# Optimization experiments

Hardware: AMD Instinct MI355X
Metric: run time of the kernel (lower is better)

Reference implementation:

```python
import jax, jax.numpy as jnp
import numpy as np

B, S, D, H = 2, 2048, 2048, 16
DH = D // H
FF = 4 * D
EPS = 1e-5


def setup_inputs() -> dict:
    key = jax.random.key(0)
    ks = jax.random.split(key, 8)
    sd = 0.02
    return {
        "hidden_states": jax.random.normal(ks[0], (B, S, D), jnp.float32),
        "ln1_w": jnp.ones((D,), jnp.float32),
        "ln1_b": jnp.zeros((D,), jnp.float32),
        "qkv_w": jax.random.normal(ks[1], (3 * D, D), jnp.float32) * sd,
        "qkv_b": jnp.zeros((3 * D,), jnp.float32),
        "dense_w": jax.random.normal(ks[2], (D, D), jnp.float32) * sd,
        "dense_b": jnp.zeros((D,), jnp.float32),
        "ln2_w": jnp.ones((D,), jnp.float32),
        "ln2_b": jnp.zeros((D,), jnp.float32),
        "fc1_w": jax.random.normal(ks[3], (FF, D), jnp.float32) * sd,
        "fc1_b": jnp.zeros((FF,), jnp.float32),
        "fc2_w": jax.random.normal(ks[4], (D, FF), jnp.float32) * sd,
        "fc2_b": jnp.zeros((D,), jnp.float32),
    }


def _layer_norm(x, w, b):
    mu = jnp.mean(x, axis=-1, keepdims=True)
    var = jnp.mean(jnp.square(x - mu), axis=-1, keepdims=True)
    return (x - mu) * jax.lax.rsqrt(var + EPS) * w + b


def _attention(x, qkv_w, qkv_b, dense_w, dense_b):
    qkv = x @ qkv_w.T + qkv_b  # [B,S,3D]
    q, k, v = jnp.split(qkv, 3, axis=-1)
    q = q.reshape(B, S, H, DH)
    k = k.reshape(B, S, H, DH)
    v = v.reshape(B, S, H, DH)
    scale = DH ** -0.5
    scores = jnp.einsum("bqhd,bkhd->bhqk", q, k) * scale
    causal = jnp.tril(jnp.ones((S, S), bool))
    scores = jnp.where(causal, scores, jnp.finfo(scores.dtype).min)
    probs = jax.nn.softmax(scores, axis=-1)
    out = jnp.einsum("bhqk,bkhd->bqhd", probs, v).reshape(B, S, D)
    return out @ dense_w.T + dense_b


def reference(hidden_states, ln1_w, ln1_b, qkv_w, qkv_b, dense_w, dense_b,
              ln2_w, ln2_b, fc1_w, fc1_b, fc2_w, fc2_b):
    residual = hidden_states
    x = _layer_norm(hidden_states, ln1_w, ln1_b)
    x = _attention(x, qkv_w, qkv_b, dense_w, dense_b) + residual
    residual = x
    h = _layer_norm(x, ln2_w, ln2_b)
    h = jax.nn.gelu(h @ fc1_w.T + fc1_b, approximate=False)
    h = h @ fc2_w.T + fc2_b
    return residual + h
```

## Files before the change

kernel.cpp:

```cpp
#include <hip/hip_runtime.h>
#include <hip/hip_bf16.h>

#define SEQ    2048
#define DMODEL 2048
#define NHEAD  16
#define DHEAD  128
#define TOK    4096
#define TD     6144
#define FFDIM  8192

typedef __attribute__((ext_vector_type(4)))  float f32x4;
typedef __attribute__((ext_vector_type(16))) float f32x16;
typedef __attribute__((ext_vector_type(8)))  short short8v;

__device__ __forceinline__ void async_ld16(const void* src, void* lds) {
  __builtin_amdgcn_global_load_lds((const __attribute__((address_space(1))) void*)src,
                                   (__attribute__((address_space(3))) void*)lds, 16, 0, 0);
}

__device__ __forceinline__ unsigned pk2(float a, float b) {
  union { __hip_bfloat16 h[2]; unsigned u; } p;
  p.h[0] = __float2bfloat16(a);
  p.h[1] = __float2bfloat16(b);
  return p.u;
}

__global__ __launch_bounds__(256) void f2bf_kernel(const float* __restrict__ in,
                                                   __hip_bfloat16* __restrict__ out, long n) {
  long i0 = ((long)blockIdx.x * 256 + threadIdx.x) * 8;
  long stride = (long)gridDim.x * 256 * 8;
  for (long i = i0; i < n; i += stride) {
    float4 a = *(const float4*)(in + i);
    float4 b = *(const float4*)(in + i + 4);
    union { __hip_bfloat16 h[8]; int4 v; } p;
    p.h[0] = __float2bfloat16(a.x); p.h[1] = __float2bfloat16(a.y);
    p.h[2] = __float2bfloat16(a.z); p.h[3] = __float2bfloat16(a.w);
    p.h[4] = __float2bfloat16(b.x); p.h[5] = __float2bfloat16(b.y);
    p.h[6] = __float2bfloat16(b.z); p.h[7] = __float2bfloat16(b.w);
    *(int4*)(out + i) = p.v;
  }
}

__global__ __launch_bounds__(256) void ln_kernel(const float* __restrict__ x,
                                                 const float* __restrict__ w,
                                                 const float* __restrict__ b,
                                                 __hip_bfloat16* __restrict__ out) {
  __shared__ float red[8];
  const int row = blockIdx.x;
  const int tid = threadIdx.x;
  const float* xr = x + (long)row * DMODEL;
  float4 v0 = ((const float4*)xr)[tid * 2];
  float4 v1 = ((const float4*)xr)[tid * 2 + 1];
  float s  = v0.x + v0.y + v0.z + v0.w + v1.x + v1.y + v1.z + v1.w;
  float ss = v0.x*v0.x + v0.y*v0.y + v0.z*v0.z + v0.w*v0.w
           + v1.x*v1.x + v1.y*v1.y + v1.z*v1.z + v1.w*v1.w;
  #pragma unroll
  for (int m = 1; m < 64; m <<= 1) { s += __shfl_xor(s, m, 64); ss += __shfl_xor(ss, m, 64); }
  if ((tid & 63) == 0) { red[tid >> 6] = s; red[4 + (tid >> 6)] = ss; }
  __syncthreads();
  s  = red[0] + red[1] + red[2] + red[3];
  ss = red[4] + red[5] + red[6] + red[7];
  const float mu = s * (1.0f / DMODEL);
  const float rs = rsqrtf(ss * (1.0f / DMODEL) - mu * mu + 1e-5f);
  float4 w0 = ((const float4*)w)[tid * 2], w1 = ((const float4*)w)[tid * 2 + 1];
  float4 b0 = ((const float4*)b)[tid * 2], b1 = ((const float4*)b)[tid * 2 + 1];
  union { __hip_bfloat16 h[8]; int4 v; } p;
  p.h[0] = __float2bfloat16((v0.x - mu) * rs * w0.x + b0.x);
  p.h[1] = __float2bfloat16((v0.y - mu) * rs * w0.y + b0.y);
  p.h[2] = __float2bfloat16((v0.z - mu) * rs * w0.z + b0.z);
  p.h[3] = __float2bfloat16((v0.w - mu) * rs * w0.w + b0.w);
  p.h[4] = __float2bfloat16((v1.x - mu) * rs * w1.x + b1.x);
  p.h[5] = __float2bfloat16((v1.y - mu) * rs * w1.y + b1.y);
  p.h[6] = __float2bfloat16((v1.z - mu) * rs * w1.z + b1.z);
  p.h[7] = __float2bfloat16((v1.w - mu) * rs * w1.w + b1.w);
  ((int4*)(out + (long)row * DMODEL))[tid] = p.v;
}

template <int MODE, int BM>
__global__ __launch_bounds__(512, 2) void gemm8p(const __hip_bfloat16* __restrict__ A,
                                                 const __hip_bfloat16* __restrict__ B,
                                                 const float* __restrict__ bias,
                                                 const float* __restrict__ resid,
                                                 void* __restrict__ outp,
                                                 int N, long K) {
  constexpr int MR     = BM / 32;
  constexpr int MH     = MR / 2;
  constexpr int A_ISS  = BM / 128;
  constexpr int ABYTES = BM * 64;
  constexpr int BUFB   = ABYTES + 16384;
  __shared__ __align__(16) char lds[4 * BUFB];

  const int tid  = threadIdx.x;
  const int lane = tid & 63;
  const int w    = tid >> 6;
  const int wr   = w >> 2, wc = w & 3;
  const long m0  = (long)blockIdx.y * BM;
  const long n0  = (long)blockIdx.x * 256;
  const int  NT  = (int)(K >> 5);

  const int srow = w * 16 + (lane >> 2);
  const int schk = lane & 3;

  auto stageA = [&](int t) {
    char* base = lds + (t & 3) * BUFB;
    #pragma unroll
    for (int i = 0; i < A_ISS; ++i) {
      int row = srow + i * 128;
      long gc = (long)t * 32 + (long)((schk ^ (row & 3)) * 8);
      async_ld16(A + (m0 + row) * K + gc, base + i * 8192 + w * 1024);
    }
  };
  auto stageB = [&](int t) {
    char* base = lds + (t & 3) * BUFB + ABYTES;
    #pragma unroll
    for (int i = 0; i < 2; ++i) {
      int row = srow + i * 128;
      long gc = (long)t * 32 + (long)((schk ^ (row & 3)) * 8);
      async_ld16(B + (n0 + row) * K + gc, base + i * 8192 + w * 1024);
    }
  };

  f32x4 acc[MR][4] = {};

  #pragma unroll
  for (int t = 0; t < 4; ++t) { stageA(t); stageB(t); }
  if constexpr (BM == 256) asm volatile("s_waitcnt vmcnt(8)\ns_barrier" ::: "memory");
  else                     asm volatile("s_waitcnt vmcnt(6)\ns_barrier" ::: "memory");

  const int c16 = lane >> 4;
  const int l15 = lane & 15;

  for (int t = 0; t < NT; ++t) {
    const int st = (t + 3 < NT) ? t + 3 : NT - 1;
    const char* bb = lds + (t & 3) * BUFB;

    stageA(st);
    short8v bfr[4], af[MH];
    #pragma unroll
    for (int n = 0; n < 4; ++n) {
      int row = wc * 64 + n * 16 + l15;
      bfr[n] = *(const short8v*)(bb + ABYTES + row * 64 + ((c16 ^ (row & 3)) << 4));
    }
    #pragma unroll
    for (int m = 0; m < MH; ++m) {
      int row = wr * (BM / 2) + m * 16 + l15;
      af[m] = *(const short8v*)(bb + row * 64 + ((c16 ^ (row & 3)) << 4));
    }
    __builtin_amdgcn_s_setprio(1);
    #pragma unroll
    for (int m = 0; m < MH; ++m)
      #pragma unroll
      for (int n = 0; n < 4; ++n)
        acc[m][n] = __builtin_amdgcn_mfma_f32_16x16x32_bf16(af[m], bfr[n], acc[m][n], 0, 0, 0);
    __builtin_amdgcn_s_setprio(0);

    stageB(st);
    #pragma unroll
    for (int m = 0; m < MH; ++m) {
      int row = wr * (BM / 2) + (MH + m) * 16 + l15;
      af[m] = *(const short8v*)(bb + row * 64 + ((c16 ^ (row & 3)) << 4));
    }
    __builtin_amdgcn_s_setprio(1);
    #pragma unroll
    for (int m = 0; m < MH; ++m)
      #pragma unroll
      for (int n = 0; n < 4; ++n)
        acc[MH + m][n] = __builtin_amdgcn_mfma_f32_16x16x32_bf16(af[m], bfr[n], acc[MH + m][n], 0, 0, 0);
    __builtin_amdgcn_s_setprio(0);

    if constexpr (BM == 256) asm volatile("s_waitcnt vmcnt(8)\ns_barrier" ::: "memory");
    else                     asm volatile("s_waitcnt vmcnt(6)\ns_barrier" ::: "memory");
  }

  const int colq = l15;
  const int rowq = (lane >> 4) * 4;
  #pragma unroll
  for (int n = 0; n < 4; ++n) {
    long col = n0 + wc * 64 + n * 16 + colq;
    float bi = bias[col];
    #pragma unroll
    for (int mi = 0; mi < MR; ++mi) {
      long row0 = m0 + wr * (BM / 2) + mi * 16 + rowq;
      #pragma unroll
      for (int j = 0; j < 4; ++j) {
        long idx = (row0 + j) * (long)N + col;
        float v = acc[mi][n][j] + bi;
        if (MODE == 0) {
          ((__hip_bfloat16*)outp)[idx] = __float2bfloat16(v);
        } else if (MODE == 1) {
          ((float*)outp)[idx] = v + resid[idx];
        } else {
          float g = 0.5f * v * (1.0f + erff(v * 0.70710678118654752f));
          ((__hip_bfloat16*)outp)[idx] = __float2bfloat16(g);
        }
      }
    }
  }
}

#define QBLK 128
#define KVB  64
#define VSTR 144
#define KBYT 16384
#define VBYT (DHEAD * VSTR)
__global__ __launch_bounds__(256, 2) void attn_kernel(const __hip_bfloat16* __restrict__ qkv,
                                                      __hip_bfloat16* __restrict__ out) {
  __shared__ __align__(16) char smem[2 * KBYT + 2 * VBYT];
  const int tid = threadIdx.x, lane = tid & 63, wid = tid >> 6;
  const int l31 = lane & 31, hi = lane >> 5;
  const int qb = (int)gridDim.x - 1 - (int)blockIdx.x;
  const int q0 = qb * QBLK;
  const int bh = blockIdx.y;
  const int bb = bh >> 4, h = bh & 15;
  const long rowbase = (long)bb * SEQ;
  const int qcol = h * DHEAD, kcol = DMODEL + h * DHEAD, vcol = 2 * DMODEL + h * DHEAD;
  const int qw0 = q0 + wid * 32;

  short8v qf[8];
  {
    const __hip_bfloat16* qp = qkv + (rowbase + qw0 + l31) * TD + qcol + hi * 8;
    #pragma unroll
    for (int kc = 0; kc < 8; ++kc) qf[kc] = *(const short8v*)(qp + kc * 16);
  }

  f32x16 o[4] = {};
  float m_ = -1e30f, l_ = 0.0f;

  const int nt = (q0 + QBLK) / KVB;

  const int kv0s = (tid >> 4) * 4;
  const int dh0s = (tid & 15) * 8;
  auto k_stage = [&](int t) {
    char* kb = smem + (t & 1) * KBYT;
    const long kvr = rowbase + (long)t * KVB;
    #pragma unroll
    for (int i = 0; i < 4; ++i) {
      int c = i * 256 + tid;
      int row = c >> 4, slot = c & 15;
      const void* src = qkv + (kvr + row) * TD + kcol + ((slot ^ (row & 7)) << 3);
      async_ld16(src, kb + i * 4096 + wid * 1024);
    }
  };
  auto v_load = [&](int t, int4* r) {
    const long kvr = rowbase + (long)t * KVB;
    #pragma unroll
    for (int i = 0; i < 4; ++i)
      r[i] = *(const int4*)(qkv + (kvr + kv0s + i) * TD + vcol + dh0s);
  };
  auto v_write = [&](int t, const int4* r) {
    char* vt = smem + 2 * KBYT + (t & 1) * VBYT;
    union { int4 v; unsigned short s[8]; } u0, u1, u2, u3;
    u0.v = r[0]; u1.v = r[1]; u2.v = r[2]; u3.v = r[3];
    #pragma unroll
    for (int dd = 0; dd < 8; ++dd) {
      int d = (dd + ((tid >> 1) & 7)) & 7;
      unsigned lo = (unsigned)u0.s[d] | ((unsigned)u1.s[d] << 16);
      unsigned hi2 = (unsigned)u2.s[d] | ((unsigned)u3.s[d] << 16);
      uint2 wv; wv.x = lo; wv.y = hi2;
      *(uint2*)(vt + (dh0s + d) * VSTR + kv0s * 2) = wv;
    }
  };

  {
    int4 vr[4];
    v_load(0, vr);
    k_stage(0);
    v_write(0, vr);
  }
  __syncthreads();

  for (int t = 0; t < nt; ++t) {
    int4 vr[4];
    const bool more = (t + 1 < nt);
    if (more) { v_load(t + 1, vr); k_stage(t + 1); }

    const int kv0 = t * KVB;
    if (kv0 <= qw0 + 31) {
      const char* Kb = smem + (t & 1) * KBYT;
      f32x16 s0 = {}, s1 = {};
      #pragma unroll
      for (int kc = 0; kc < 8; ++kc) {
        const int colb = kc * 32 + hi * 16;
        const int r0 = l31, r1 = 32 + l31;
        short8v k0 = *(const short8v*)(Kb + r0 * 256 + (colb ^ ((r0 & 7) << 4)));
        short8v k1 = *(const short8v*)(Kb + r1 * 256 + (colb ^ ((r0 & 7) << 4)));
        s0 = __builtin_amdgcn_mfma_f32_32x32x16_bf16(k0, qf[kc], s0, 0, 0, 0);
        s1 = __builtin_amdgcn_mfma_f32_32x32x16_bf16(k1, qf[kc], s1, 0, 0, 0);
      }
      const float scale = 0.08838834764831845f;
      float sv[32];
      #pragma unroll
      for (int r = 0; r < 16; ++r) { sv[r] = s0[r] * scale; sv[16 + r] = s1[r] * scale; }
      const int qg = qw0 + l31;
      if (kv0 + KVB - 1 > qw0) {
        #pragma unroll
        for (int r = 0; r < 16; ++r) {
          int kvr_ = kv0 + (r & 3) + 8 * (r >> 2) + 4 * hi;
          if (kvr_ > qg)      sv[r]      = -1e30f;
          if (kvr_ + 32 > qg) sv[16 + r] = -1e30f;
        }
      }
      float pmax = sv[0];
      #pragma unroll
      for (int r = 1; r < 32; ++r) pmax = fmaxf(pmax, sv[r]);
      pmax = fmaxf(pmax, __shfl_xor(pmax, 32, 64));
      float mn = fmaxf(m_, pmax);
      float alpha = __expf(m_ - mn);
      m_ = mn;
      l_ *= alpha;
      #pragma unroll
      for (int d = 0; d < 4; ++d)
        #pragma unroll
        for (int r = 0; r < 16; ++r) o[d][r] *= alpha;
      float rsum = 0.0f;
      #pragma unroll
      for (int r = 0; r < 32; ++r) { sv[r] = __expf(sv[r] - m_); rsum += sv[r]; }
      l_ += rsum + __shfl_xor(rsum, 32, 64);
      int pa_[4][4];
      #pragma unroll
      for (int kc = 0; kc < 4; ++kc) {
        int ba = 16 * (kc >> 1) + 8 * (kc & 1);
        unsigned wA0 = pk2(sv[ba + 0], sv[ba + 1]);
        unsigned wA1 = pk2(sv[ba + 2], sv[ba + 3]);
        unsigned wB0 = pk2(sv[ba + 4], sv[ba + 5]);
        unsigned wB1 = pk2(sv[ba + 6], sv[ba + 7]);
        unsigned z0 = (unsigned)__shfl_xor((int)(hi ? wA0 : wB0), 32, 64);
        unsigned z1 = (unsigned)__shfl_xor((int)(hi ? wA1 : wB1), 32, 64);
        pa_[kc][0] = hi ? (int)z0 : (int)wA0;
        pa_[kc][1] = hi ? (int)z1 : (int)wA1;
        pa_[kc][2] = hi ? (int)wB0 : (int)z0;
        pa_[kc][3] = hi ? (int)wB1 : (int)z1;
      }
      const char* Vt = smem + 2 * KBYT + (t & 1) * VBYT;
      #pragma unroll
      for (int dht = 0; dht < 4; ++dht) {
        const int dh = dht * 32 + l31;
        short8v vf[4];
        #pragma unroll
        for (int kc = 0; kc < 4; ++kc)
          vf[kc] = *(const short8v*)(Vt + dh * VSTR + kc * 32 + hi * 16);
        #pragma unroll
        for (int kc = 0; kc < 4; ++kc) {
          union { int i[4]; short8v v; } bv;
          bv.i[0] = pa_[kc][0]; bv.i[1] = pa_[kc][1];
          bv.i[2] = pa_[kc][2]; bv.i[3] = pa_[kc][3];
          o[dht] = __builtin_amdgcn_mfma_f32_32x32x16_bf16(vf[kc], bv.v, o[dht], 0, 0, 0);
        }
      }
    }
    if (more) v_write(t + 1, vr);
    __syncthreads();
  }

  const float linv = 1.0f / l_;
  const long orow = (rowbase + qw0 + l31) * DMODEL + h * DHEAD;
  #pragma unroll
  for (int dht = 0; dht < 4; ++dht)
    #pragma unroll
    for (int rg = 0; rg < 4; ++rg) {
      union { __hip_bfloat16 hh[4]; uint2 u; } pk;
      #pragma unroll
      for (int i = 0; i < 4; ++i) pk.hh[i] = __float2bfloat16(o[dht][rg * 4 + i] * linv);
      *(uint2*)(out + orow + dht * 32 + 8 * rg + 4 * hi) = pk.u;
    }
}

extern "C" void kernel_launch(void* const* d_in, const int* in_sizes, int n_in,
                              void* d_out, int out_size, void* d_ws, size_t ws_size,
                              hipStream_t stream) {
  const float* hidden  = (const float*)d_in[0];
  const float* ln1w    = (const float*)d_in[1];
  const float* ln1b    = (const float*)d_in[2];
  const float* qkvw    = (const float*)d_in[3];
  const float* qkvb    = (const float*)d_in[4];
  const float* densew  = (const float*)d_in[5];
  const float* denseb  = (const float*)d_in[6];
  const float* ln2w    = (const float*)d_in[7];
  const float* ln2b    = (const float*)d_in[8];
  const float* fc1w    = (const float*)d_in[9];
  const float* fc1b    = (const float*)d_in[10];
  const float* fc2w    = (const float*)d_in[11];
  const float* fc2b    = (const float*)d_in[12];

  char* ws = (char*)d_ws;
  size_t off = 0;
  auto alloc = [&](size_t bytes) { char* p = ws + off; off += (bytes + 255) & ~(size_t)255; return p; };
  __hip_bfloat16* xbf    = (__hip_bfloat16*)alloc((size_t)TOK * DMODEL * 2);
  __hip_bfloat16* wqkv   = (__hip_bfloat16*)alloc((size_t)TD * DMODEL * 2);
  __hip_bfloat16* wdense = (__hip_bfloat16*)alloc((size_t)DMODEL * DMODEL * 2);
  __hip_bfloat16* wfc1   = (__hip_bfloat16*)alloc((size_t)FFDIM * DMODEL * 2);
  __hip_bfloat16* wfc2   = (__hip_bfloat16*)alloc((size_t)DMODEL * FFDIM * 2);
  __hip_bfloat16* big    = (__hip_bfloat16*)alloc((size_t)TOK * FFDIM * 2);
  float*          x2     = (float*)alloc((size_t)TOK * DMODEL * 4);
  __hip_bfloat16* qkvbuf  = big;
  __hip_bfloat16* attnout = big + (size_t)TOK * TD;
  __hip_bfloat16* gelubuf = big;

  f2bf_kernel<<<1024, 256, 0, stream>>>(qkvw,   wqkv,   (long)TD * DMODEL);
  f2bf_kernel<<<1024, 256, 0, stream>>>(densew, wdense, (long)DMODEL * DMODEL);
  f2bf_kernel<<<1024, 256, 0, stream>>>(fc1w,   wfc1,   (long)FFDIM * DMODEL);
  f2bf_kernel<<<1024, 256, 0, stream>>>(fc2w,   wfc2,   (long)DMODEL * FFDIM);

  ln_kernel<<<TOK, 256, 0, stream>>>(hidden, ln1w, ln1b, xbf);
  gemm8p<0, 256><<<dim3(TD / 256, TOK / 256), 512, 0, stream>>>(xbf, wqkv, qkvb, nullptr, qkvbuf, TD, DMODEL);
  attn_kernel<<<dim3(SEQ / QBLK, 2 * NHEAD), 256, 0, stream>>>(qkvbuf, attnout);
  gemm8p<1, 128><<<dim3(DMODEL / 256, TOK / 128), 512, 0, stream>>>(attnout, wdense, denseb, hidden, x2, DMODEL, DMODEL);
  ln_kernel<<<TOK, 256, 0, stream>>>(x2, ln2w, ln2b, xbf);
  gemm8p<2, 256><<<dim3(FFDIM / 256, TOK / 256), 512, 0, stream>>>(xbf, wfc1, fc1b, nullptr, gelubuf, FFDIM, DMODEL);
  gemm8p<1, 128><<<dim3(DMODEL / 256, TOK / 128), 512, 0, stream>>>(gelubuf, wfc2, fc2b, x2, (float*)d_out, DMODEL, FFDIM);
}
```

Baseline: 744.0 us.

## Add finely interleaved 256x256 GEMM kernel for QKV and FC1 projections

Introduces a new 256x256-tile bf16 GEMM with double-buffered LDS, in which async global-to-LDS loads for quarter tiles are interleaved between MFMA blocks. Priority hints and explicit barriers and waitcnts keep memory traffic overlapped with matrix math. The new kernel replaces gemm8p for the QKV and FC1 projections. It uses 128KB of LDS per block and a hand-tuned barrier schedule, which may limit occupancy and could be fragile.

```diff
diff --git a/kernel.cpp b/kernel.cpp
--- a/kernel.cpp
+++ b/kernel.cpp
@@ -76,6 +76,139 @@
   ((int4*)(out + (long)row * DMODEL))[tid] = p.v;
 }
 
+#define G2_BAR()    asm volatile("s_barrier" ::: "memory")
+#define G2_BARLG()  asm volatile("s_barrier\ns_waitcnt lgkmcnt(0)" ::: "memory")
+#define G2_VM6()    asm volatile("s_waitcnt vmcnt(6)\ns_barrier" ::: "memory")
+#define G2_VM0()    asm volatile("s_waitcnt vmcnt(0)\ns_barrier" ::: "memory")
+
+#define READ_A(BB, MH) \
+  _Pragma("unroll") \
+  for (int m = 0; m < 4; ++m) { \
+    int row = wr * 128 + (MH) * 64 + m * 16 + l15; \
+    _Pragma("unroll") \
+    for (int kk = 0; kk < 2; ++kk) \
+      af[m][kk] = *(const short8v*)((BB) + row * 128 + ((((kk << 2) | c16) ^ (row & 7)) << 4)); \
+  }
+#define READ_B(BB, NB) \
+  _Pragma("unroll") \
+  for (int n = 0; n < 2; ++n) { \
+    int row = wc * 64 + ((NB) + n) * 16 + l15; \
+    _Pragma("unroll") \
+    for (int kk = 0; kk < 2; ++kk) \
+      bf[(NB) + n][kk] = *(const short8v*)((BB) + 32768 + row * 128 + ((((kk << 2) | c16) ^ (row & 7)) << 4)); \
+  }
+#define MFMA_BLK(MH, NB) \
+  __builtin_amdgcn_s_setprio(1); \
+  _Pragma("unroll") \
+  for (int m = 0; m < 4; ++m) \
+    _Pragma("unroll") \
+    for (int n = 0; n < 2; ++n) \
+      _Pragma("unroll") \
+      for (int kk = 0; kk < 2; ++kk) \
+        acc[(MH) * 4 + m][(NB) + n] = __builtin_amdgcn_mfma_f32_16x16x32_bf16( \
+            af[m][kk], bf[(NB) + n][kk], acc[(MH) * 4 + m][(NB) + n], 0, 0, 0); \
+  __builtin_amdgcn_s_setprio(0);
+
+template <int MODE>
+__global__ __launch_bounds__(512, 2) void gemm256(const __hip_bfloat16* __restrict__ A,
+                                                  const __hip_bfloat16* __restrict__ B,
+                                                  const float* __restrict__ bias,
+                                                  const float* __restrict__ resid,
+                                                  void* __restrict__ outp,
+                                                  int N, long K) {
+  __shared__ __align__(16) char lds[131072];
+  const int tid = threadIdx.x;
+  const int lane = tid & 63, w = tid >> 6;
+  const int wr = w >> 2, wc = w & 3;
+  const int l15 = lane & 15, c16 = lane >> 4;
+  const long m0 = (long)blockIdx.y * 256;
+  const long n0 = (long)blockIdx.x * 256;
+  const int NT = (int)(K >> 6);
+  const int NI = NT >> 1;
+
+  auto stA2 = [&](int t, int par) {
+    char* base = lds + (t & 1) * 65536;
+    #pragma unroll
+    for (int j = 0; j < 2; ++j) {
+      int q = 2 * j + par;
+      int row = q * 64 + (tid >> 3);
+      long col = (long)t * 64 + (((tid & 7) ^ (row & 7)) << 3);
+      async_ld16(A + (m0 + row) * K + col, base + q * 8192 + w * 1024);
+    }
+  };
+  auto stB2 = [&](int t, int half) {
+    char* base = lds + (t & 1) * 65536 + 32768;
+    #pragma unroll
+    for (int j = 0; j < 2; ++j) {
+      int row = half * 128 + j * 64 + (tid >> 3);
+      long col = (long)t * 64 + (((tid & 7) ^ (row & 7)) << 3);
+      async_ld16(B + (n0 + row) * K + col, base + half * 16384 + j * 8192 + w * 1024);
+    }
+  };
+
+  f32x4 acc[8][4] = {};
+  short8v af[4][2], bf[4][2];
+  const char* b0 = lds;
+  const char* b1 = lds + 65536;
+
+  stA2(0, 0); stB2(0, 0); stA2(0, 1); stB2(0, 1);
+  stA2(1, 0); stB2(1, 0); stA2(1, 1);
+  G2_VM6();
+
+  for (int i = 0; i < NI; ++i) {
+    const bool lastit = (i == NI - 1);
+    READ_A(b0, 0); READ_B(b0, 0);
+    stB2(2 * i + 1, 1);
+    G2_BARLG(); MFMA_BLK(0, 0); G2_BAR();
+    READ_B(b0, 2);
+    if (!lastit) stA2(2 * i + 2, 0);
+    G2_BARLG(); MFMA_BLK(0, 2); G2_BAR();
+    READ_A(b0, 1);
+    if (!lastit) stB2(2 * i + 2, 0);
+    G2_BARLG(); MFMA_BLK(1, 2); G2_BAR();
+    if (!lastit) stA2(2 * i + 2, 1);
+    G2_BARLG(); MFMA_BLK(1, 0);
+    if (lastit) { G2_VM0(); } else { G2_VM6(); }
+    READ_A(b1, 0); READ_B(b1, 0);
+    if (!lastit) stB2(2 * i + 2, 1);
+    G2_BARLG(); MFMA_BLK(0, 0); G2_BAR();
+    READ_B(b1, 2);
+    if (!lastit) stA2(2 * i + 3, 0);
+    G2_BARLG(); MFMA_BLK(0, 2); G2_BAR();
+    READ_A(b1, 1);
+    if (!lastit) stB2(2 * i + 3, 0);
+    G2_BARLG(); MFMA_BLK(1, 2); G2_BAR();
+    if (!lastit) stA2(2 * i + 3, 1);
+    G2_BARLG(); MFMA_BLK(1, 0);
+    if (lastit) { G2_BAR(); } else { G2_VM6(); }
+  }
+
+  const int colq = l15;
+  const int rowq = c16 * 4;
+  #pragma unroll
+  for (int n = 0; n < 4; ++n) {
+    long col = n0 + wc * 64 + n * 16 + colq;
+    float bi = bias[col];
+    #pragma unroll
+    for (int mi = 0; mi < 8; ++mi) {
+      long row0 = m0 + wr * 128 + mi * 16 + rowq;
+      #pragma unroll
+      for (int j = 0; j < 4; ++j) {
+        long idx = (row0 + j) * (long)N + col;
+        float v = acc[mi][n][j] + bi;
+        if (MODE == 0) {
+          ((__hip_bfloat16*)outp)[idx] = __float2bfloat16(v);
+        } else if (MODE == 1) {
+          ((float*)outp)[idx] = v + resid[idx];
+        } else {
+          float g = 0.5f * v * (1.0f + erff(v * 0.70710678118654752f));
+          ((__hip_bfloat16*)outp)[idx] = __float2bfloat16(g);
+        }
+      }
+    }
+  }
+}
+
 template <int MODE, int BM>
 __global__ __launch_bounds__(512, 2) void gemm8p(const __hip_bfloat16* __restrict__ A,
                                                  const __hip_bfloat16* __restrict__ B,
@@ -402,10 +535,10 @@
   f2bf_kernel<<<1024, 256, 0, stream>>>(fc2w,   wfc2,   (long)DMODEL * FFDIM);
 
   ln_kernel<<<TOK, 256, 0, stream>>>(hidden, ln1w, ln1b, xbf);
-  gemm8p<0, 256><<<dim3(TD / 256, TOK / 256), 512, 0, stream>>>(xbf, wqkv, qkvb, nullptr, qkvbuf, TD, DMODEL);
+  gemm256<0><<<dim3(TD / 256, TOK / 256), 512, 0, stream>>>(xbf, wqkv, qkvb, nullptr, qkvbuf, TD, DMODEL);
   attn_kernel<<<dim3(SEQ / QBLK, 2 * NHEAD), 256, 0, stream>>>(qkvbuf, attnout);
   gemm8p<1, 128><<<dim3(DMODEL / 256, TOK / 128), 512, 0, stream>>>(attnout, wdense, denseb, hidden, x2, DMODEL, DMODEL);
   ln_kernel<<<TOK, 256, 0, stream>>>(x2, ln2w, ln2b, xbf);
-  gemm8p<2, 256><<<dim3(FFDIM / 256, TOK / 256), 512, 0, stream>>>(xbf, wfc1, fc1b, nullptr, gelubuf, FFDIM, DMODEL);
+  gemm256<2><<<dim3(FFDIM / 256, TOK / 256), 512, 0, stream>>>(xbf, wfc1, fc1b, nullptr, gelubuf, FFDIM, DMODEL);
   gemm8p<1, 128><<<dim3(DMODEL / 256, TOK / 128), 512, 0, stream>>>(gelubuf, wfc2, fc2b, x2, (float*)d_out, DMODEL, FFDIM);
 }
```

Measured after the change: 728.8 us. 1.02x faster.
